# Optimization experiments

Measured on AMD Instinct MI355X. Metric: run time of the kernel, lower is better.

## Reference

```python
import jax, jax.numpy as jnp
import numpy as np

MAX_DISP = 4          # init kwarg
WIN = 2 * MAX_DISP + 1  # 9 -> 81 displacement offsets
CHUNK = 16            # hardcoded channel chunk size in the torch module


def setup_inputs() -> dict:
    key = jax.random.key(0)
    k1, k2 = jax.random.split(key)
    B, C, H, W = 8, 128, 96, 160
    x1 = jax.random.normal(k1, (B, C, H, W), dtype=jnp.float32)
    x2 = jax.random.normal(k2, (B, C, H, W), dtype=jnp.float32)
    return {"x1": x1, "x2": x2}


def reference(x1, x2):
    B, C, H, W = x2.shape
    pad = MAX_DISP
    # replicate padding == torch F.pad mode='replicate' == jnp 'edge'
    x2p = jnp.pad(x2, ((0, 0), (0, 0), (pad, pad), (pad, pad)), mode="edge")
    # offsets in the same row-major (dy outer, dx inner) order as the torch loops
    dy, dx = jnp.meshgrid(jnp.arange(-pad, pad + 1), jnp.arange(-pad, pad + 1), indexing="ij")
    offsets = jnp.stack([dy.ravel(), dx.ravel()], axis=1)  # [81, 2]
    num_chunks = -(-C // CHUNK)  # ceil(C/16); with C%16==0 chunk-mean == total-sum/num_chunks

    def body(carry, off):
        # shifted window of x2: x2p[:, :, pad+dy : pad+dy+H, pad+dx : pad+dx+W]
        sl = jax.lax.dynamic_slice(x2p, (0, 0, pad + off[0], pad + off[1]), (B, C, H, W))
        return carry, jnp.sum(x1 * sl, axis=1)  # [B, H, W]

    _, corr = jax.lax.scan(body, None, offsets)  # [81, B, H, W]
    corr = jnp.transpose(corr, (1, 0, 2, 3))     # [B, 81, H, W]
    return corr / jnp.asarray(num_chunks, corr.dtype)
```

## Files before the change

### kernel.cpp

```cpp
#include <hip/hip_runtime.h>
#include <cstdint>

#define BB 8
#define CC 128
#define HH 96
#define WW 160
#define HWsz (HH * WW)
#define TH 8
#define TW 32
#define CSTEP 8
#define HALO_H 16
#define SW 48
#define CI_WORDS (HALO_H * SW)
#define BUF_WORDS (CSTEP * CI_WORDS)
#define NWAVES 9
#define NTHREADS (NWAVES * 64)
#define NSLOTS (CSTEP * HALO_H)
#define NCHUNKS (CC / CSTEP)
#define NBLOCKS (BB * (HH / TH) * (WW / TW))

__device__ __forceinline__ void g2l_dword(const float* g, float* l) {
  __builtin_amdgcn_global_load_lds((const __attribute__((address_space(1))) void*)g,
                                   (__attribute__((address_space(3))) void*)l,
                                   4, 0, 0);
}

__device__ __forceinline__ void stage_chunk(const float* __restrict__ src, float* dst,
                                            int h0, int w0, int lane, int wvu) {
  for (int slot = wvu; slot < NSLOTS; slot += NWAVES) {
    const int ci  = slot >> 4;
    const int row = slot & 15;
    int gh = h0 + row - 4; gh = gh < 0 ? 0 : (gh > HH - 1 ? HH - 1 : gh);
    const int cl = lane ^ ((row & 3) << 2);
    int gw = w0 + cl - 4; gw = gw < 0 ? 0 : (gw > WW - 1 ? WW - 1 : gw);
    if (lane < SW)
      g2l_dword(src + (ci * HH + gh) * WW + gw, dst + ci * CI_WORDS + row * SW);
  }
}

extern "C" __global__ void __launch_bounds__(NTHREADS, 2)
corr81_kernel(const float* __restrict__ x1, const float* __restrict__ x2,
              float* __restrict__ out)
{
  __shared__ __align__(16) float lds[2][BUF_WORDS];

  const int tid  = threadIdx.x;
  const int wv   = tid >> 6;
  const int wvu  = __builtin_amdgcn_readfirstlane(wv);
  const int lane = tid & 63;
  const int r    = lane >> 3;
  const int j    = lane & 7;

  const int bid0 = blockIdx.x;
  const int bid  = (bid0 & 7) * (NBLOCKS / 8) + (bid0 >> 3);

  const int wt = bid % (WW / TW);
  const int ht = (bid / (WW / TW)) % (HH / TH);
  const int b  = bid / ((WW / TW) * (HH / TH));
  const int h0 = ht * TH;
  const int w0 = wt * TW;

  const int R = r + wv;
  const int m = R & 3;
  int A[3];
#pragma unroll
  for (int t = 0; t < 3; ++t)
    A[t] = R * SW + 4 * ((j + t) ^ m);

  const float* x2b = x2 + b * (CC * HWsz);
  const float* x1p = x1 + b * (CC * HWsz) + (h0 + r) * WW + (w0 + 4 * j);

  float acc[9][4];
#pragma unroll
  for (int d = 0; d < 9; ++d)
#pragma unroll
    for (int p = 0; p < 4; ++p) acc[d][p] = 0.f;

  stage_chunk(x2b, &lds[0][0], h0, w0, lane, wvu);
  __syncthreads();

#pragma unroll 1
  for (int chunk = 0; chunk < NCHUNKS; ++chunk) {
    if (chunk + 1 < NCHUNKS)
      stage_chunk(x2b + (chunk + 1) * (CSTEP * HWsz),
                  &lds[(chunk + 1) & 1][0], h0, w0, lane, wvu);

    const float* lb = &lds[0][0];
#pragma unroll
    for (int ci = 0; ci < CSTEP; ++ci) {
      const float4 a4 = *(const float4*)(x1p + ci * HWsz);
      const float av[4] = {a4.x, a4.y, a4.z, a4.w};
      float w12[12];
#pragma unroll
      for (int t = 0; t < 3; ++t) {
        const float4 f = *(const float4*)(lb + A[t] + ci * CI_WORDS);
        w12[4*t+0] = f.x; w12[4*t+1] = f.y; w12[4*t+2] = f.z; w12[4*t+3] = f.w;
      }
#pragma unroll
      for (int d = 0; d < 9; ++d)
#pragma unroll
        for (int p = 0; p < 4; ++p)
          acc[d][p] = fmaf(av[p], w12[d + p], acc[d][p]);
    }

    x1p += CSTEP * HWsz;
    const int flip = (chunk & 1) ? -BUF_WORDS : BUF_WORDS;
    A[0] += flip; A[1] += flip; A[2] += flip;
    __syncthreads();
  }

  float* op = out + ((b * 81 + wv * 9) * HH + (h0 + r)) * WW + (w0 + 4 * j);
#pragma unroll
  for (int d = 0; d < 9; ++d) {
    float4 v;
    v.x = acc[d][0] * 0.125f;
    v.y = acc[d][1] * 0.125f;
    v.z = acc[d][2] * 0.125f;
    v.w = acc[d][3] * 0.125f;
    *(float4*)(op + d * HWsz) = v;
  }
}

extern "C" void kernel_launch(void* const* d_in, const int* in_sizes, int n_in,
                              void* d_out, int out_size, void* d_ws, size_t ws_size,
                              hipStream_t stream) {
  const float* x1 = (const float*)d_in[0];
  const float* x2 = (const float*)d_in[1];
  float* out = (float*)d_out;
  corr81_kernel<<<dim3(NBLOCKS), dim3(NTHREADS), 0, stream>>>(x1, x2, out);
}
```

Measured before the change: 248.6 us.

## Split each tile into nine single-wave blocks with per-wave LDS pipelining

Each 9-wave workgroup becomes nine independent 64-thread blocks, one per dy row of displacements. Each wave stages only its own 8-row x2 halo through a double-buffered LDS buffer and orders async loads with vmcnt waits instead of __syncthreads. It also prefetches x1 into registers one chunk ahead and halves the channel step to 4. This removes cross-wave barriers and raises scheduling flexibility, but each block now loads its own overlapping halo, so x2 global/L2 traffic grows about 9x/2x, and per-block launch overhead increases.

```diff
diff --git a/kernel.cpp b/kernel.cpp
--- a/kernel.cpp
+++ b/kernel.cpp
@@ -8,16 +8,13 @@
 #define HWsz (HH * WW)
 #define TH 8
 #define TW 32
-#define CSTEP 8
-#define HALO_H 16
-#define SW 48
-#define CI_WORDS (HALO_H * SW)
-#define BUF_WORDS (CSTEP * CI_WORDS)
-#define NWAVES 9
-#define NTHREADS (NWAVES * 64)
-#define NSLOTS (CSTEP * HALO_H)
-#define NCHUNKS (CC / CSTEP)
-#define NBLOCKS (BB * (HH / TH) * (WW / TW))
+#define CSTEP 4
+#define NCH (CC / CSTEP)
+#define SW2 64
+#define CI_WORDS (TH * SW2)
+#define X2W (CSTEP * CI_WORDS)
+#define NTILES (BB * (HH / TH) * (WW / TW))
+#define NBLOCKS (NTILES * 9)
 
 __device__ __forceinline__ void g2l_dword(const float* g, float* l) {
   __builtin_amdgcn_global_load_lds((const __attribute__((address_space(1))) void*)g,
@@ -25,50 +22,46 @@
                                    4, 0, 0);
 }
 
-__device__ __forceinline__ void stage_chunk(const float* __restrict__ src, float* dst,
-                                            int h0, int w0, int lane, int wvu) {
-  for (int slot = wvu; slot < NSLOTS; slot += NWAVES) {
-    const int ci  = slot >> 4;
-    const int row = slot & 15;
-    int gh = h0 + row - 4; gh = gh < 0 ? 0 : (gh > HH - 1 ? HH - 1 : gh);
-    const int cl = lane ^ ((row & 3) << 2);
-    int gw = w0 + cl - 4; gw = gw < 0 ? 0 : (gw > WW - 1 ? WW - 1 : gw);
-    if (lane < SW)
-      g2l_dword(src + (ci * HH + gh) * WW + gw, dst + ci * CI_WORDS + row * SW);
-  }
-}
-
-extern "C" __global__ void __launch_bounds__(NTHREADS, 2)
+extern "C" __global__ void __launch_bounds__(64, 1)
 corr81_kernel(const float* __restrict__ x1, const float* __restrict__ x2,
               float* __restrict__ out)
 {
-  __shared__ __align__(16) float lds[2][BUF_WORDS];
+  __shared__ __align__(16) float lds[2 * X2W];
 
-  const int tid  = threadIdx.x;
-  const int wv   = tid >> 6;
-  const int wvu  = __builtin_amdgcn_readfirstlane(wv);
-  const int lane = tid & 63;
+  const int lane = threadIdx.x;
   const int r    = lane >> 3;
   const int j    = lane & 7;
 
   const int bid0 = blockIdx.x;
   const int bid  = (bid0 & 7) * (NBLOCKS / 8) + (bid0 >> 3);
+  const int tile = bid / 9;
+  const int wv   = bid - 9 * tile;
+  const int wt   = tile % (WW / TW);
+  const int ht   = (tile / (WW / TW)) % (HH / TH);
+  const int b    = tile / ((WW / TW) * (HH / TH));
+  const int h0   = ht * TH;
+  const int w0   = wt * TW;
 
-  const int wt = bid % (WW / TW);
-  const int ht = (bid / (WW / TW)) % (HH / TH);
-  const int b  = bid / ((WW / TW) * (HH / TH));
-  const int h0 = ht * TH;
-  const int w0 = wt * TW;
+  int gw[4];
+#pragma unroll
+  for (int g = 0; g < 4; ++g) {
+    const int cl = lane ^ (g << 2);
+    int gwv = w0 + cl - 4;
+    gwv = gwv < 0 ? 0 : (gwv > WW - 1 ? WW - 1 : gwv);
+    gw[g] = gwv;
+  }
 
-  const int R = r + wv;
-  const int m = R & 3;
-  int A[3];
+  int sb2[32];
 #pragma unroll
-  for (int t = 0; t < 3; ++t)
-    A[t] = R * SW + 4 * ((j + t) ^ m);
+  for (int i = 0; i < 32; ++i) {
+    const int ci  = i >> 3;
+    const int row = i & 7;
+    int gh = h0 + wv + row - 4; gh = gh < 0 ? 0 : (gh > HH - 1 ? HH - 1 : gh);
+    sb2[i] = (ci * HH + gh) * WW;
+  }
 
-  const float* x2b = x2 + b * (CC * HWsz);
-  const float* x1p = x1 + b * (CC * HWsz) + (h0 + r) * WW + (w0 + 4 * j);
+  const float* x2b = x2 + (size_t)b * CC * HWsz;
+  const float* x1c = x1 + (size_t)b * CC * HWsz + (size_t)(h0 + r) * WW + (w0 + 4 * j);
 
   float acc[9][4];
 #pragma unroll
@@ -76,40 +69,71 @@
 #pragma unroll
     for (int p = 0; p < 4; ++p) acc[d][p] = 0.f;
 
-  stage_chunk(x2b, &lds[0][0], h0, w0, lane, wvu);
-  __syncthreads();
+  const int m  = r & 3;
+  const int B0 = r * SW2 + (((j + 0) ^ m) << 2);
+  const int B1 = r * SW2 + (((j + 1) ^ m) << 2);
+  const int B2 = r * SW2 + (((j + 2) ^ m) << 2);
+
+#define STAGE(DST, SRC)                                                      \
+  if (lane < 48) {                                                           \
+    _Pragma("unroll")                                                        \
+    for (int i = 0; i < 32; ++i)                                             \
+      g2l_dword((SRC) + sb2[i] + gw[i & 3], (DST) + i * 64);                 \
+  }
+
+#define COMPUTE(XB)                                                          \
+  {                                                                          \
+    _Pragma("unroll")                                                        \
+    for (int ci = 0; ci < CSTEP; ++ci) {                                     \
+      const float av[4] = {pf[ci].x, pf[ci].y, pf[ci].z, pf[ci].w};          \
+      const float4 f0 = *(const float4*)((XB) + B0 + ci * CI_WORDS);         \
+      const float4 f1 = *(const float4*)((XB) + B1 + ci * CI_WORDS);         \
+      const float4 f2 = *(const float4*)((XB) + B2 + ci * CI_WORDS);         \
+      const float w12[12] = {f0.x, f0.y, f0.z, f0.w, f1.x, f1.y, f1.z,       \
+                             f1.w, f2.x, f2.y, f2.z, f2.w};                  \
+      _Pragma("unroll")                                                      \
+      for (int d = 0; d < 9; ++d)                                            \
+        _Pragma("unroll")                                                    \
+        for (int p = 0; p < 4; ++p)                                          \
+          acc[d][p] = fmaf(av[p], w12[d + p], acc[d][p]);                    \
+    }                                                                        \
+  }
+
+  float4 pf[4];
+
+  STAGE(&lds[0], x2b)
+#pragma unroll
+  for (int q = 0; q < CSTEP; ++q)
+    pf[q] = *(const float4*)(x1c + (size_t)q * HWsz);
 
 #pragma unroll 1
-  for (int chunk = 0; chunk < NCHUNKS; ++chunk) {
-    if (chunk + 1 < NCHUNKS)
-      stage_chunk(x2b + (chunk + 1) * (CSTEP * HWsz),
-                  &lds[(chunk + 1) & 1][0], h0, w0, lane, wvu);
+  for (int k = 0; k < NCH - 1; ++k) {
+    __builtin_amdgcn_sched_barrier(0);
+    {
+      const float* s2 = x2b + (size_t)(k + 1) * (CSTEP * HWsz);
+      float* d2 = &lds[((k + 1) & 1) * X2W];
+      STAGE(d2, s2)
+    }
+    __builtin_amdgcn_sched_barrier(0);
+    asm volatile("s_waitcnt vmcnt(32)" ::: "memory");
+    __builtin_amdgcn_sched_barrier(0);
 
-    const float* lb = &lds[0][0];
+    COMPUTE(&lds[(k & 1) * X2W])
+
+    {
+      const float* xn = x1c + (size_t)(k + 1) * (CSTEP * HWsz);
 #pragma unroll
-    for (int ci = 0; ci < CSTEP; ++ci) {
-      const float4 a4 = *(const float4*)(x1p + ci * HWsz);
-      const float av[4] = {a4.x, a4.y, a4.z, a4.w};
-      float w12[12];
-#pragma unroll
-      for (int t = 0; t < 3; ++t) {
-        const float4 f = *(const float4*)(lb + A[t] + ci * CI_WORDS);
-        w12[4*t+0] = f.x; w12[4*t+1] = f.y; w12[4*t+2] = f.z; w12[4*t+3] = f.w;
-      }
-#pragma unroll
-      for (int d = 0; d < 9; ++d)
-#pragma unroll
-        for (int p = 0; p < 4; ++p)
-          acc[d][p] = fmaf(av[p], w12[d + p], acc[d][p]);
+      for (int q = 0; q < CSTEP; ++q)
+        pf[q] = *(const float4*)(xn + (size_t)q * HWsz);
     }
-
-    x1p += CSTEP * HWsz;
-    const int flip = (chunk & 1) ? -BUF_WORDS : BUF_WORDS;
-    A[0] += flip; A[1] += flip; A[2] += flip;
-    __syncthreads();
   }
 
-  float* op = out + ((b * 81 + wv * 9) * HH + (h0 + r)) * WW + (w0 + 4 * j);
+  __builtin_amdgcn_sched_barrier(0);
+  asm volatile("s_waitcnt vmcnt(0)" ::: "memory");
+  __builtin_amdgcn_sched_barrier(0);
+  COMPUTE(&lds[((NCH - 1) & 1) * X2W])
+
+  float* op = out + (((size_t)b * 81 + (size_t)wv * 9) * HH + (h0 + r)) * WW + (w0 + 4 * j);
 #pragma unroll
   for (int d = 0; d < 9; ++d) {
     float4 v;
@@ -117,7 +141,7 @@
     v.y = acc[d][1] * 0.125f;
     v.z = acc[d][2] * 0.125f;
     v.w = acc[d][3] * 0.125f;
-    *(float4*)(op + d * HWsz) = v;
+    *(float4*)(op + (size_t)d * HWsz) = v;
   }
 }
 
@@ -127,5 +151,5 @@
   const float* x1 = (const float*)d_in[0];
   const float* x2 = (const float*)d_in[1];
   float* out = (float*)d_out;
-  corr81_kernel<<<dim3(NBLOCKS), dim3(NTHREADS), 0, stream>>>(x1, x2, out);
+  corr81_kernel<<<dim3(NBLOCKS), dim3(64), 0, stream>>>(x1, x2, out);
 }
```

Measured after the change: 276.2 us. 11.1% more time.
